# Kernel tuning notes

Hardware: AMD Instinct MI355X
Metric: run time of the kernel (lower is better)

Reference implementation:

```python
import jax, jax.numpy as jnp
import numpy as np

C_S, C_Z, H = 384, 128, 8
HD = C_S // H
EPS = 1e-5

def _layernorm(x, g, b):
    mu = jnp.mean(x, axis=-1, keepdims=True)
    var = jnp.mean((x - mu) ** 2, axis=-1, keepdims=True)
    return (x - mu) * jax.lax.rsqrt(var + EPS) * g + b

def setup_inputs() -> dict:
    key = jax.random.key(0)
    ks = jax.random.split(key, 12)
    B, L = 1, 768
    sc = lambda d: 1.0 / np.sqrt(d)
    return {
        "single": jax.random.normal(ks[0], (B, L, C_S), jnp.float32),
        "pair": jax.random.normal(ks[1], (B, L, L, C_Z), jnp.float32),
        "g_s": jnp.ones((C_S,), jnp.float32),
        "b_s": jnp.zeros((C_S,), jnp.float32),
        "g_z": jnp.ones((C_Z,), jnp.float32),
        "b_z": jnp.zeros((C_Z,), jnp.float32),
        "Wq": jax.random.normal(ks[2], (C_S, C_S), jnp.float32) * sc(C_S),
        "Wk": jax.random.normal(ks[3], (C_S, C_S), jnp.float32) * sc(C_S),
        "Wv": jax.random.normal(ks[4], (C_S, C_S), jnp.float32) * sc(C_S),
        "Wb": jax.random.normal(ks[5], (C_Z, H), jnp.float32) * sc(C_Z),
        "Wo": jax.random.normal(ks[6], (C_S, C_S), jnp.float32) * sc(C_S),
        "bo": jnp.zeros((C_S,), jnp.float32),
        "Wg": jax.random.normal(ks[7], (C_S, C_S), jnp.float32) * sc(C_S),
        "bg": jnp.zeros((C_S,), jnp.float32),
    }

def reference(single, pair, g_s, b_s, g_z, b_z, Wq, Wk, Wv, Wb, Wo, bo, Wg, bg):
    B, L, _ = single.shape
    s = _layernorm(single, g_s, b_s)                      # [B,L,C_S]
    z = _layernorm(pair, g_z, b_z)                        # [B,L,L,C_Z]
    q = (s @ Wq.T).reshape(B, L, H, HD)
    k = (s @ Wk.T).reshape(B, L, H, HD)
    v = (s @ Wv.T).reshape(B, L, H, HD)
    attn = jnp.einsum('bihd,bjhd->bhij', q, k) / np.sqrt(HD)
    bias = jnp.einsum('bijz,zh->bhij', z, Wb)             # pair bias per head
    attn = jax.nn.softmax(attn + bias, axis=-1)
    out = jnp.einsum('bhij,bjhd->bihd', attn, v).reshape(B, L, C_S)
    gate = jax.nn.sigmoid(s @ Wg.T + bg)
    return single + gate * (out @ Wo.T + bo)
```

## Files before the change

### kernel.cpp

```cpp
#include <hip/hip_runtime.h>
#include <hip/hip_bf16.h>
#include <cstdint>
#include <cstddef>

#define LSEQ 768
#define CS 384
#define CZ 128
#define NH 8
#define HD 48
#define LL (LSEQ*LSEQ)

static constexpr float EPS = 1e-5f;
static constexpr float QK_SCALE = 0.14433756729740643f;

typedef __attribute__((ext_vector_type(8))) short bf16x8;
typedef __attribute__((ext_vector_type(4))) float f32x4;

__device__ __forceinline__ short f2bf_s(float f){
  unsigned int u = __float_as_uint(f);
  unsigned int r = u + 0x7fffu + ((u >> 16) & 1u);
  return (short)(r >> 16);
}

__global__ void k_ln_single(const float* __restrict__ single,
                            const float* __restrict__ g,
                            const float* __restrict__ b,
                            float* __restrict__ s_out){
  const int i = blockIdx.x;
  const int lane = threadIdx.x;
  const float* row = single + i*CS;
  float x[6];
  float sum = 0.f;
#pragma unroll
  for(int e=0;e<6;e++){ x[e] = row[lane + 64*e]; sum += x[e]; }
#pragma unroll
  for(int m=32;m>=1;m>>=1) sum += __shfl_xor(sum, m, 64);
  const float mu = sum * (1.f/CS);
  float vs = 0.f;
#pragma unroll
  for(int e=0;e<6;e++){ float d = x[e]-mu; vs += d*d; }
#pragma unroll
  for(int m=32;m>=1;m>>=1) vs += __shfl_xor(vs, m, 64);
  const float rs = rsqrtf(vs*(1.f/CS) + EPS);
#pragma unroll
  for(int e=0;e<6;e++){
    int c = lane + 64*e;
    s_out[i*CS + c] = (x[e]-mu)*rs*g[c] + b[c];
  }
}

__global__ __launch_bounds__(256,4) void k_pair_bias(
    const float* __restrict__ pair,
    const float* __restrict__ g_z,
    const float* __restrict__ b_z,
    const float* __restrict__ Wb,
    float* __restrict__ bias){
  const int t = threadIdx.x;
  const int lane = t & 63;
  const int wave = t >> 6;
  const int sub  = lane >> 4;
  const int lg   = lane & 15;
  const int z0   = lg*8;

  float wb_r[64], gz[8], bz[8];
#pragma unroll
  for(int zz=0; zz<8; zz++){
    gz[zz] = g_z[z0+zz];
    bz[zz] = b_z[z0+zz];
#pragma unroll
    for(int h=0; h<NH; h++) wb_r[zz*8+h] = Wb[(z0+zz)*NH + h];
  }
  const int hmap = 4*(lg&1) + (lg&2) + ((lg>>2)&1);

  const int ngroups = LL/16;
  for(int gidx = blockIdx.x; gidx < ngroups; gidx += gridDim.x){
    const int r = gidx*16 + wave*4 + sub;
    const float4 u0 = *(const float4*)(pair + (size_t)r*CZ + z0);
    const float4 u1 = *(const float4*)(pair + (size_t)r*CZ + z0 + 4);
    float x[8] = {u0.x,u0.y,u0.z,u0.w,u1.x,u1.y,u1.z,u1.w};
    float sum=0.f, sq=0.f;
#pragma unroll
    for(int e=0;e<8;e++){ sum += x[e]; sq += x[e]*x[e]; }
#pragma unroll
    for(int m=1;m<16;m<<=1){ sum += __shfl_xor(sum,m,64); sq += __shfl_xor(sq,m,64); }
    const float mu = sum*(1.f/CZ);
    const float rs = rsqrtf(sq*(1.f/CZ) - mu*mu + EPS);
    float acc[8];
#pragma unroll
    for(int h=0;h<8;h++) acc[h]=0.f;
#pragma unroll
    for(int e=0;e<8;e++){
      const float zn = (x[e]-mu)*rs*gz[e] + bz[e];
#pragma unroll
      for(int h=0;h<8;h++) acc[h] += zn*wb_r[e*8+h];
    }
    float k1[4];
    {
      const bool hi = lg & 1;
#pragma unroll
      for(int j=0;j<4;j++){
        float send = hi ? acc[j] : acc[j+4];
        float recv = __shfl_xor(send, 1, 64);
        k1[j] = (hi ? acc[j+4] : acc[j]) + recv;
      }
    }
    float k2[2];
    {
      const bool hi = lg & 2;
#pragma unroll
      for(int j=0;j<2;j++){
        float send = hi ? k1[j] : k1[j+2];
        float recv = __shfl_xor(send, 2, 64);
        k2[j] = (hi ? k1[j+2] : k1[j]) + recv;
      }
    }
    float k3;
    {
      const bool hi = lg & 4;
      float send = hi ? k2[0] : k2[1];
      float recv = __shfl_xor(send, 4, 64);
      k3 = (hi ? k2[1] : k2[0]) + recv;
    }
    k3 += __shfl_xor(k3, 8, 64);
    if(lg < 8) bias[(size_t)hmap*LL + r] = k3;
  }
}

__global__ __launch_bounds__(256) void k_qkvg(
    const float* __restrict__ s,
    const float* __restrict__ Wq, const float* __restrict__ Wk,
    const float* __restrict__ Wv, const float* __restrict__ Wg,
    const float* __restrict__ bg,
    float* __restrict__ q, float* __restrict__ k,
    float* __restrict__ v, float* __restrict__ gate){
  const int which = blockIdx.z;
  const float* W = (which==0)?Wq : (which==1)?Wk : (which==2)?Wv : Wg;
  float* out = (which==0)?q : (which==1)?k : (which==2)?v : gate;
  __shared__ float As[16][65];
  __shared__ float Bs[16][65];
  const int t = threadIdx.x;
  const int m0 = blockIdx.x*64;
  const int n0 = blockIdx.y*64;
  const int tx = t & 15, ty = t >> 4;
  float acc[4][4] = {};
  for(int k0=0;k0<CS;k0+=16){
#pragma unroll
    for(int e=0;e<4;e++){
      int idx = t + e*256;
      int kk = idx & 15, mm = idx >> 4;
      As[kk][mm] = s[(m0+mm)*CS + k0 + kk];
      Bs[kk][mm] = W[(n0+mm)*CS + k0 + kk];
    }
    __syncthreads();
#pragma unroll
    for(int kk=0;kk<16;kk++){
      float a[4], bb[4];
#pragma unroll
      for(int rr=0;rr<4;rr++) a[rr]=As[kk][ty+16*rr];
#pragma unroll
      for(int cc=0;cc<4;cc++) bb[cc]=Bs[kk][tx+16*cc];
#pragma unroll
      for(int rr=0;rr<4;rr++)
#pragma unroll
        for(int cc=0;cc<4;cc++) acc[rr][cc] += a[rr]*bb[cc];
    }
    __syncthreads();
  }
#pragma unroll
  for(int rr=0;rr<4;rr++){
    int m = m0 + ty + 16*rr;
#pragma unroll
    for(int cc=0;cc<4;cc++){
      int n = n0 + tx + 16*cc;
      float val = acc[rr][cc];
      if(which==3) val = 1.f/(1.f + __expf(-(val + bg[n])));
      out[m*CS+n] = val;
    }
  }
}

__global__ __launch_bounds__(256) void k_flash(
    const float* __restrict__ q, const float* __restrict__ k,
    const float* __restrict__ v, const float* __restrict__ bias,
    float* __restrict__ attno){
  const int h  = blockIdx.y;
  const int i0 = blockIdx.x * 16;
  const int t  = threadIdx.x;
  const int w    = t >> 6;
  const int lane = t & 63;
  const int ln   = lane & 15;
  const int quad = lane >> 4;

  __shared__ float S_lds[4][16][34];
  __shared__ float O_lds[4][16][48];
  __shared__ float ml_lds[4][2][16];

  bf16x8 aq0, aq1;
  {
    const float* qrow = q + (size_t)(i0 + ln)*CS + h*HD;
#pragma unroll
    for(int e=0;e<8;e++) aq0[e] = f2bf_s(qrow[quad*8 + e] * QK_SCALE);
    if(quad < 2){
#pragma unroll
      for(int e=0;e<8;e++) aq1[e] = f2bf_s(qrow[32 + quad*8 + e] * QK_SCALE);
    } else {
#pragma unroll
      for(int e=0;e<8;e++) aq1[e] = 0;
    }
  }

  float m_r[4], l_r[4];
  f32x4 o[3];
#pragma unroll
  for(int r=0;r<4;r++){ m_r[r] = -INFINITY; l_r[r] = 0.f; }
#pragma unroll
  for(int db=0;db<3;db++) o[db] = (f32x4){0.f,0.f,0.f,0.f};

  for(int jt=0; jt<6; jt++){
    const int j0 = w*192 + jt*32;
    f32x4 s_f[2];
#pragma unroll
    for(int jb=0;jb<2;jb++){
      const float* krow = k + (size_t)(j0 + jb*16 + ln)*CS + h*HD;
      bf16x8 bk0, bk1;
#pragma unroll
      for(int e=0;e<8;e++) bk0[e] = f2bf_s(krow[quad*8 + e]);
      if(quad < 2){
#pragma unroll
        for(int e=0;e<8;e++) bk1[e] = f2bf_s(krow[32 + quad*8 + e]);
      } else {
#pragma unroll
        for(int e=0;e<8;e++) bk1[e] = 0;
      }
      f32x4 acc = (f32x4){0.f,0.f,0.f,0.f};
      acc = __builtin_amdgcn_mfma_f32_16x16x32_bf16(aq0, bk0, acc, 0,0,0);
      acc = __builtin_amdgcn_mfma_f32_16x16x32_bf16(aq1, bk1, acc, 0,0,0);
      s_f[jb] = acc;
    }
    float sv[2][4];
#pragma unroll
    for(int jb=0;jb<2;jb++)
#pragma unroll
      for(int r=0;r<4;r++)
        sv[jb][r] = s_f[jb][r] +
          bias[(size_t)h*LL + (size_t)(i0 + quad*4 + r)*LSEQ + j0 + jb*16 + ln];
    float tmax[4];
#pragma unroll
    for(int r=0;r<4;r++) tmax[r] = fmaxf(sv[0][r], sv[1][r]);
#pragma unroll
    for(int r=0;r<4;r++)
#pragma unroll
      for(int m=1;m<16;m<<=1) tmax[r] = fmaxf(tmax[r], __shfl_xor(tmax[r], m, 64));
    float alpha[4];
#pragma unroll
    for(int r=0;r<4;r++){
      const float mn = fmaxf(m_r[r], tmax[r]);
      alpha[r] = __expf(m_r[r] - mn);
      m_r[r] = mn;
    }
    float p[2][4], tsum[4];
#pragma unroll
    for(int r=0;r<4;r++){
      p[0][r] = __expf(sv[0][r] - m_r[r]);
      p[1][r] = __expf(sv[1][r] - m_r[r]);
      tsum[r] = p[0][r] + p[1][r];
    }
#pragma unroll
    for(int r=0;r<4;r++)
#pragma unroll
      for(int m=1;m<16;m<<=1) tsum[r] += __shfl_xor(tsum[r], m, 64);
#pragma unroll
    for(int r=0;r<4;r++) l_r[r] = l_r[r]*alpha[r] + tsum[r];
#pragma unroll
    for(int db=0;db<3;db++)
#pragma unroll
      for(int r=0;r<4;r++) o[db][r] *= alpha[r];
#pragma unroll
    for(int jb=0;jb<2;jb++)
#pragma unroll
      for(int r=0;r<4;r++) S_lds[w][quad*4+r][jb*16+ln] = p[jb][r];
    bf16x8 ap;
#pragma unroll
    for(int e=0;e<8;e++) ap[e] = f2bf_s(S_lds[w][ln][quad*8+e]);
#pragma unroll
    for(int db=0;db<3;db++){
      bf16x8 bv;
#pragma unroll
      for(int jj=0;jj<8;jj++)
        bv[jj] = f2bf_s(v[(size_t)(j0 + quad*8 + jj)*CS + h*HD + db*16 + ln]);
      o[db] = __builtin_amdgcn_mfma_f32_16x16x32_bf16(ap, bv, o[db], 0,0,0);
    }
  }

#pragma unroll
  for(int db=0;db<3;db++)
#pragma unroll
    for(int r=0;r<4;r++) O_lds[w][quad*4+r][db*16+ln] = o[db][r];
  if(ln == 0){
#pragma unroll
    for(int r=0;r<4;r++){
      ml_lds[w][0][quad*4+r] = m_r[r];
      ml_lds[w][1][quad*4+r] = l_r[r];
    }
  }
  __syncthreads();
#pragma unroll
  for(int e=0;e<3;e++){
    const int idx = t + e*256;
    const int row = idx / 48, d = idx % 48;
    float M = ml_lds[0][0][row];
#pragma unroll
    for(int ww=1;ww<4;ww++) M = fmaxf(M, ml_lds[ww][0][row]);
    float L = 0.f, O = 0.f;
#pragma unroll
    for(int ww=0;ww<4;ww++){
      const float f = __expf(ml_lds[ww][0][row] - M);
      L += ml_lds[ww][1][row] * f;
      O += O_lds[ww][row][d] * f;
    }
    attno[(size_t)(i0+row)*CS + h*HD + d] = O / L;
  }
}

__global__ __launch_bounds__(256) void k_final(
    const float* __restrict__ attno, const float* __restrict__ Wo,
    const float* __restrict__ bo, const float* __restrict__ single,
    const float* __restrict__ gate, float* __restrict__ out){
  __shared__ float As[16][65];
  __shared__ float Bs[16][65];
  const int t = threadIdx.x;
  const int m0 = blockIdx.x*64;
  const int n0 = blockIdx.y*64;
  const int tx = t & 15, ty = t >> 4;
  float acc[4][4] = {};
  for(int k0=0;k0<CS;k0+=16){
#pragma unroll
    for(int e=0;e<4;e++){
      int idx = t + e*256;
      int kk = idx & 15, mm = idx >> 4;
      As[kk][mm] = attno[(m0+mm)*CS + k0 + kk];
      Bs[kk][mm] = Wo[(n0+mm)*CS + k0 + kk];
    }
    __syncthreads();
#pragma unroll
    for(int kk=0;kk<16;kk++){
      float a[4], bb[4];
#pragma unroll
      for(int rr=0;rr<4;rr++) a[rr]=As[kk][ty+16*rr];
#pragma unroll
      for(int cc=0;cc<4;cc++) bb[cc]=Bs[kk][tx+16*cc];
#pragma unroll
      for(int rr=0;rr<4;rr++)
#pragma unroll
        for(int cc=0;cc<4;cc++) acc[rr][cc] += a[rr]*bb[cc];
    }
    __syncthreads();
  }
#pragma unroll
  for(int rr=0;rr<4;rr++){
    int m = m0 + ty + 16*rr;
#pragma unroll
    for(int cc=0;cc<4;cc++){
      int n = n0 + tx + 16*cc;
      float val = acc[rr][cc] + bo[n];
      out[m*CS+n] = single[m*CS+n] + gate[m*CS+n]*val;
    }
  }
}

extern "C" void kernel_launch(void* const* d_in, const int* in_sizes, int n_in,
                              void* d_out, int out_size, void* d_ws, size_t ws_size,
                              hipStream_t stream){
  (void)in_sizes; (void)n_in; (void)out_size; (void)ws_size;
  const float* single = (const float*)d_in[0];
  const float* pair   = (const float*)d_in[1];
  const float* g_s    = (const float*)d_in[2];
  const float* b_s    = (const float*)d_in[3];
  const float* g_z    = (const float*)d_in[4];
  const float* b_z    = (const float*)d_in[5];
  const float* Wq     = (const float*)d_in[6];
  const float* Wk     = (const float*)d_in[7];
  const float* Wv     = (const float*)d_in[8];
  const float* Wb     = (const float*)d_in[9];
  const float* Wo     = (const float*)d_in[10];
  const float* bo     = (const float*)d_in[11];
  const float* Wg     = (const float*)d_in[12];
  const float* bg     = (const float*)d_in[13];
  float* out = (float*)d_out;

  float* ws     = (float*)d_ws;
  float* bias   = ws;
  float* s      = ws + 4718592;
  float* q      = s  + 294912;
  float* k      = q  + 294912;
  float* v      = k  + 294912;
  float* gate   = v  + 294912;
  float* attno  = gate + 294912;

  hipLaunchKernelGGL(k_ln_single, dim3(768),     dim3(64),  0, stream, single, g_s, b_s, s);
  hipLaunchKernelGGL(k_pair_bias, dim3(3072),    dim3(256), 0, stream, pair, g_z, b_z, Wb, bias);
  hipLaunchKernelGGL(k_qkvg,      dim3(12,6,4),  dim3(256), 0, stream, s, Wq, Wk, Wv, Wg, bg, q, k, v, gate);
  hipLaunchKernelGGL(k_flash,     dim3(48,8),    dim3(256), 0, stream, q, k, v, bias, attno);
  hipLaunchKernelGGL(k_final,     dim3(12,6),    dim3(256), 0, stream, attno, Wo, bo, single, gate, out);
}
```

Baseline: 528.4 us.

## Store Q/K/V as bf16 with transposed V and vectorized MFMA operand loads

The projection kernel now writes Q (pre-scaled), K and a transposed V directly as bf16, so the flash kernel loads MFMA operands as 16-byte vectors instead of converting scalar fp32 loads. The P tile is stored in LDS as bf16 and read back as one vector. This cuts global traffic and conversion work in the attention loop. The transposed V writes in the projection epilogue are strided and uncoalesced.

```diff
diff --git a/kernel.cpp b/kernel.cpp
--- a/kernel.cpp
+++ b/kernel.cpp
@@ -13,13 +13,14 @@
 static constexpr float EPS = 1e-5f;
 static constexpr float QK_SCALE = 0.14433756729740643f;
 
+typedef unsigned short u16;
 typedef __attribute__((ext_vector_type(8))) short bf16x8;
 typedef __attribute__((ext_vector_type(4))) float f32x4;
 
-__device__ __forceinline__ short f2bf_s(float f){
+__device__ __forceinline__ u16 f2bf_s(float f){
   unsigned int u = __float_as_uint(f);
   unsigned int r = u + 0x7fffu + ((u >> 16) & 1u);
-  return (short)(r >> 16);
+  return (u16)(r >> 16);
 }
 
 __global__ void k_ln_single(const float* __restrict__ single,
@@ -131,11 +132,10 @@
     const float* __restrict__ Wq, const float* __restrict__ Wk,
     const float* __restrict__ Wv, const float* __restrict__ Wg,
     const float* __restrict__ bg,
-    float* __restrict__ q, float* __restrict__ k,
-    float* __restrict__ v, float* __restrict__ gate){
+    u16* __restrict__ qb, u16* __restrict__ kb,
+    u16* __restrict__ vT, float* __restrict__ gate){
   const int which = blockIdx.z;
   const float* W = (which==0)?Wq : (which==1)?Wk : (which==2)?Wv : Wg;
-  float* out = (which==0)?q : (which==1)?k : (which==2)?v : gate;
   __shared__ float As[16][65];
   __shared__ float Bs[16][65];
   const int t = threadIdx.x;
@@ -173,15 +173,17 @@
     for(int cc=0;cc<4;cc++){
       int n = n0 + tx + 16*cc;
       float val = acc[rr][cc];
-      if(which==3) val = 1.f/(1.f + __expf(-(val + bg[n])));
-      out[m*CS+n] = val;
+      if(which==0)      qb[m*CS+n] = f2bf_s(val*QK_SCALE);
+      else if(which==1) kb[m*CS+n] = f2bf_s(val);
+      else if(which==2) vT[(size_t)n*LSEQ + m] = f2bf_s(val);
+      else              gate[m*CS+n] = 1.f/(1.f + __expf(-(val + bg[n])));
     }
   }
 }
 
 __global__ __launch_bounds__(256) void k_flash(
-    const float* __restrict__ q, const float* __restrict__ k,
-    const float* __restrict__ v, const float* __restrict__ bias,
+    const u16* __restrict__ qb, const u16* __restrict__ kb,
+    const u16* __restrict__ vT, const float* __restrict__ bias,
     float* __restrict__ attno){
   const int h  = blockIdx.y;
   const int i0 = blockIdx.x * 16;
@@ -191,22 +193,17 @@
   const int ln   = lane & 15;
   const int quad = lane >> 4;
 
-  __shared__ float S_lds[4][16][34];
+  __shared__ u16  S_lds[4][16][32];
   __shared__ float O_lds[4][16][48];
   __shared__ float ml_lds[4][2][16];
 
+  const bf16x8 zf = {0,0,0,0,0,0,0,0};
+
   bf16x8 aq0, aq1;
   {
-    const float* qrow = q + (size_t)(i0 + ln)*CS + h*HD;
-#pragma unroll
-    for(int e=0;e<8;e++) aq0[e] = f2bf_s(qrow[quad*8 + e] * QK_SCALE);
-    if(quad < 2){
-#pragma unroll
-      for(int e=0;e<8;e++) aq1[e] = f2bf_s(qrow[32 + quad*8 + e] * QK_SCALE);
-    } else {
-#pragma unroll
-      for(int e=0;e<8;e++) aq1[e] = 0;
-    }
+    const u16* qrow = qb + (size_t)(i0 + ln)*CS + h*HD;
+    aq0 = *(const bf16x8*)(qrow + quad*8);
+    aq1 = (quad < 2) ? *(const bf16x8*)(qrow + 32 + quad*8) : zf;
   }
 
   float m_r[4], l_r[4];
@@ -221,17 +218,9 @@
     f32x4 s_f[2];
 #pragma unroll
     for(int jb=0;jb<2;jb++){
-      const float* krow = k + (size_t)(j0 + jb*16 + ln)*CS + h*HD;
-      bf16x8 bk0, bk1;
-#pragma unroll
-      for(int e=0;e<8;e++) bk0[e] = f2bf_s(krow[quad*8 + e]);
-      if(quad < 2){
-#pragma unroll
-        for(int e=0;e<8;e++) bk1[e] = f2bf_s(krow[32 + quad*8 + e]);
-      } else {
-#pragma unroll
-        for(int e=0;e<8;e++) bk1[e] = 0;
-      }
+      const u16* krow = kb + (size_t)(j0 + jb*16 + ln)*CS + h*HD;
+      bf16x8 bk0 = *(const bf16x8*)(krow + quad*8);
+      bf16x8 bk1 = (quad < 2) ? *(const bf16x8*)(krow + 32 + quad*8) : zf;
       f32x4 acc = (f32x4){0.f,0.f,0.f,0.f};
       acc = __builtin_amdgcn_mfma_f32_16x16x32_bf16(aq0, bk0, acc, 0,0,0);
       acc = __builtin_amdgcn_mfma_f32_16x16x32_bf16(aq1, bk1, acc, 0,0,0);
@@ -278,16 +267,11 @@
 #pragma unroll
     for(int jb=0;jb<2;jb++)
 #pragma unroll
-      for(int r=0;r<4;r++) S_lds[w][quad*4+r][jb*16+ln] = p[jb][r];
-    bf16x8 ap;
-#pragma unroll
-    for(int e=0;e<8;e++) ap[e] = f2bf_s(S_lds[w][ln][quad*8+e]);
+      for(int r=0;r<4;r++) S_lds[w][quad*4+r][jb*16+ln] = f2bf_s(p[jb][r]);
+    bf16x8 ap = *(const bf16x8*)&S_lds[w][ln][quad*8];
 #pragma unroll
     for(int db=0;db<3;db++){
-      bf16x8 bv;
-#pragma unroll
-      for(int jj=0;jj<8;jj++)
-        bv[jj] = f2bf_s(v[(size_t)(j0 + quad*8 + jj)*CS + h*HD + db*16 + ln]);
+      bf16x8 bv = *(const bf16x8*)(vT + (size_t)(h*HD + db*16 + ln)*LSEQ + j0 + quad*8);
       o[db] = __builtin_amdgcn_mfma_f32_16x16x32_bf16(ap, bv, o[db], 0,0,0);
     }
   }
@@ -391,15 +375,15 @@
   float* ws     = (float*)d_ws;
   float* bias   = ws;
   float* s      = ws + 4718592;
-  float* q      = s  + 294912;
-  float* k      = q  + 294912;
-  float* v      = k  + 294912;
-  float* gate   = v  + 294912;
+  float* gate   = s + 294912;
   float* attno  = gate + 294912;
+  u16*   qb     = (u16*)(ws + 4718592 + 3*294912);
+  u16*   kb     = qb + 294912;
+  u16*   vT     = kb + 294912;
 
   hipLaunchKernelGGL(k_ln_single, dim3(768),     dim3(64),  0, stream, single, g_s, b_s, s);
   hipLaunchKernelGGL(k_pair_bias, dim3(3072),    dim3(256), 0, stream, pair, g_z, b_z, Wb, bias);
-  hipLaunchKernelGGL(k_qkvg,      dim3(12,6,4),  dim3(256), 0, stream, s, Wq, Wk, Wv, Wg, bg, q, k, v, gate);
-  hipLaunchKernelGGL(k_flash,     dim3(48,8),    dim3(256), 0, stream, q, k, v, bias, attno);
+  hipLaunchKernelGGL(k_qkvg,      dim3(12,6,4),  dim3(256), 0, stream, s, Wq, Wk, Wv, Wg, bg, qb, kb, vT, gate);
+  hipLaunchKernelGGL(k_flash,     dim3(48,8),    dim3(256), 0, stream, qb, kb, vT, bias, attno);
   hipLaunchKernelGGL(k_final,     dim3(12,6),    dim3(256), 0, stream, attno, Wo, bo, single, gate, out);
 }
```

Measured after the change: 520.4 us. About the same (-1.5%).
